# Kernel optimization log

Measured on AMD Instinct MI355X. Metric: run time of the kernel, lower is better.

Reference implementation:

```python
import jax, jax.numpy as jnp
import numpy as np

N_NODES = 50000
N_EDGES = 800000
N_GRAPHS = 512
IN_C, HID, OUT_C = 128, 256, 16


def _mlp(h, w1, b1, w2, b2):
    # PyG-style 2-layer MLP: Linear -> ReLU -> Linear (plain last layer)
    return jax.nn.relu(h @ w1 + b1) @ w2 + b2


def setup_inputs() -> dict:
    key = jax.random.key(0)
    ks = jax.random.split(key, 16)
    x = jax.random.normal(ks[0], (N_NODES, IN_C), dtype=jnp.float32)
    edge_index = jax.random.randint(ks[1], (2, N_EDGES), 0, N_NODES, dtype=jnp.int64)
    batch = jnp.sort(jax.random.randint(ks[2], (N_NODES,), 0, N_GRAPHS, dtype=jnp.int64))

    def lin(k, fan_in, fan_out):
        s = 1.0 / np.sqrt(fan_in)
        return jax.random.uniform(k, (fan_in, fan_out), jnp.float32, -s, s)

    inp = {"x": x, "edge_index": edge_index, "batch": batch}
    dims = [(IN_C, HID), (HID, HID), (HID, HID)]
    ki = 3
    for li, (din, dh) in enumerate(dims):
        inp[f"c{li}_w1"] = lin(ks[ki], din, dh); ki += 1
        inp[f"c{li}_b1"] = jnp.zeros((dh,), jnp.float32)
        inp[f"c{li}_w2"] = lin(ks[ki], dh, dh); ki += 1
        inp[f"c{li}_b2"] = jnp.zeros((dh,), jnp.float32)
    inp["out_w1"] = lin(ks[ki], HID, HID); ki += 1
    inp["out_b1"] = jnp.zeros((HID,), jnp.float32)
    inp["out_w2"] = lin(ks[ki], HID, OUT_C); ki += 1
    inp["out_b2"] = jnp.zeros((OUT_C,), jnp.float32)
    return inp


def reference(x, edge_index, batch,
              c0_w1, c0_b1, c0_w2, c0_b2,
              c1_w1, c1_b1, c1_w2, c1_b2,
              c2_w1, c2_b1, c2_w2, c2_b2,
              out_w1, out_b1, out_w2, out_b2):
    src, dst = edge_index[0], edge_index[1]
    params = [(c0_w1, c0_b1, c0_w2, c0_b2),
              (c1_w1, c1_b1, c1_w2, c1_b2),
              (c2_w1, c2_b1, c2_w2, c2_b2)]
    h = x
    for (w1, b1, w2, b2) in params:
        # GINConv with eps=0: MLP(x + sum_{j in N(i)} x_j)
        agg = jax.ops.segment_sum(h[src], dst, num_segments=N_NODES)
        h = _mlp(h + agg, w1, b1, w2, b2)
        h = jax.nn.relu(h)
        # dropout: identity (eval mode)
    # global mean pool over graphs
    sums = jax.ops.segment_sum(h, batch, num_segments=N_GRAPHS)
    counts = jax.ops.segment_sum(jnp.ones((N_NODES,), h.dtype), batch, num_segments=N_GRAPHS)
    pooled = sums / jnp.maximum(counts, 1.0)[:, None]
    return _mlp(pooled, out_w1, out_b1, out_w2, out_b2)
```

## Files before the change

### kernel.cpp

```cpp
#include <hip/hip_runtime.h>

#define N_NODES 50000
#define N_EDGES 800000
#define N_GRAPHS 512
#define IN_C 128
#define HID 256
#define OUT_C 16

typedef __attribute__((ext_vector_type(8))) short short8;
typedef __attribute__((ext_vector_type(4))) float f32x4;

__device__ __forceinline__ float bf2f(unsigned short u) {
    return __uint_as_float(((unsigned int)u) << 16);
}
__device__ __forceinline__ unsigned short f2bf(float f) {
    unsigned int u = __float_as_uint(f);
    u += 0x7fff + ((u >> 16) & 1);
    return (unsigned short)(u >> 16);
}

#define PLANE_ELEMS ((long)N_NODES * 32)

struct PrepArgs {
    const float* x;
    const float* w[6];
    ushort* xbf;
    ushort* wt[6];
    int* deg;
    float* sums;
};

__global__ __launch_bounds__(256) void prep_kernel(PrepArgs a) {
    const int X4    = N_NODES * IN_C / 4;
    const int TW    = IN_C * HID;
    const int TH    = HID * HID;
    const int TBASE = X4;
    const int TEND  = TBASE + TW + 5 * TH;
    const int D4    = N_NODES / 4;
    const int DBASE = TEND;
    const int SBASE = DBASE + D4;
    const int S4    = N_GRAPHS * HID / 4;
    const long total = (long)SBASE + S4;

    long stride = (long)gridDim.x * blockDim.x;
    for (long i = (long)blockIdx.x * blockDim.x + threadIdx.x; i < total; i += stride) {
        if (i < X4) {
            float4 v = ((const float4*)a.x)[i];
            ushort4 o;
            o.x = f2bf(v.x); o.y = f2bf(v.y); o.z = f2bf(v.z); o.w = f2bf(v.w);
            long e = i * 4;
            int node = (int)(e >> 7);
            int col  = (int)(e & 127);
            long off = (long)(col >> 5) * PLANE_ELEMS + (long)node * 32 + (col & 31);
            *(ushort4*)(a.xbf + off) = o;
        } else if (i < TEND) {
            long r = i - TBASE;
            int wi, shift;
            long off;
            if (r < TW) { wi = 0; shift = 7; off = r; }
            else { r -= TW; wi = 1 + (int)(r / TH); shift = 8; off = r % TH; }
            int n = (int)(off >> shift);
            int k = (int)(off - ((long)n << shift));
            a.wt[wi][off] = f2bf(a.w[wi][(long)k * HID + n]);
        } else if (i < SBASE) {
            ((int4*)a.deg)[i - DBASE] = make_int4(0, 0, 0, 0);
        } else {
            ((float4*)a.sums)[i - SBASE] = make_float4(0.f, 0.f, 0.f, 0.f);
        }
    }
}

__global__ void deg_rank_kernel(const int* __restrict__ dst, int* __restrict__ deg,
                                int* __restrict__ rank) {
    int e = blockIdx.x * blockDim.x + threadIdx.x;
    if (e < N_EDGES) rank[e] = atomicAdd(&deg[dst[e]], 1);
}

__global__ __launch_bounds__(256) void scan_block(const int* __restrict__ deg,
                                                  int* __restrict__ partial,
                                                  int* __restrict__ blockSums) {
    __shared__ int s[256];
    int t = threadIdx.x;
    int i = blockIdx.x * 256 + t;
    int v = (i < N_NODES) ? deg[i] : 0;
    s[t] = v;
    __syncthreads();
    #pragma unroll
    for (int off = 1; off < 256; off <<= 1) {
        int add = (t >= off) ? s[t - off] : 0;
        __syncthreads();
        s[t] += add;
        __syncthreads();
    }
    if (i < N_NODES) partial[i] = s[t] - v;
    if (t == 255) blockSums[blockIdx.x] = s[255];
}

__global__ __launch_bounds__(256) void add_offsets_fused(
    const int* __restrict__ partial, const int* __restrict__ blockSums,
    int* __restrict__ rowptr, int nb) {
    __shared__ int s[256];
    __shared__ int myOff;
    int t = threadIdx.x;
    int v = (t < nb) ? blockSums[t] : 0;
    s[t] = v;
    __syncthreads();
    #pragma unroll
    for (int off = 1; off < 256; off <<= 1) {
        int add = (t >= off) ? s[t - off] : 0;
        __syncthreads();
        s[t] += add;
        __syncthreads();
    }
    if (t == blockIdx.x) myOff = s[t] - v;
    __syncthreads();
    int i = blockIdx.x * 256 + t;
    if (i < N_NODES) rowptr[i] = partial[i] + myOff;
    if (i == 0) rowptr[N_NODES] = N_EDGES;
}

#define NSHARD 8
#define SHARD_SZ ((N_NODES + NSHARD - 1) / NSHARD)
#define EDGES_PER_BLK 2048

__global__ __launch_bounds__(256) void scatter_edges_sharded(
    const int* __restrict__ src, const int* __restrict__ dst,
    const int* __restrict__ rank, const int* __restrict__ rowptr,
    int* __restrict__ srcSorted) {
    int b = blockIdx.x;
    int shard = b & 7;
    int chunk = b >> 3;
    int lo = shard * SHARD_SZ;
    int hi = lo + SHARD_SZ;
    int base = chunk * EDGES_PER_BLK + threadIdx.x;
    #pragma unroll
    for (int u = 0; u < EDGES_PER_BLK / 256; ++u) {
        int e = base + u * 256;
        if (e < N_EDGES) {
            int d = dst[e];
            if (d >= lo && d < hi)
                srcSorted[rowptr[d] + rank[e]] = src[e];
        }
    }
}

template <int C>
__global__ __launch_bounds__(256) void gin_aggregate_planar(
    const ushort* __restrict__ hp,
    const int* __restrict__ rowptr,
    const int* __restrict__ srcIdx,
    ushort* __restrict__ out)
{
    constexpr int NC  = C / 32;
    constexpr int PER = 8 / NC;

    int b  = blockIdx.x;
    int x8 = b & 7;
    int chunk   = x8 / PER;
    int nodeblk = (b >> 3) * PER + (x8 & (PER - 1));

    int lane = threadIdx.x & 63;
    int wave = threadIdx.x >> 6;
    int grp  = lane >> 2;
    int l    = lane & 3;
    int node = nodeblk * 64 + wave * 16 + grp;
    if (node >= N_NODES) return;

    const ushort* plane = hp + (long)chunk * PLANE_ELEMS + l * 8;

    float acc[8];
    {
        short8 sv = *(const short8*)(plane + (long)node * 32);
        #pragma unroll
        for (int v = 0; v < 8; ++v) acc[v] = bf2f((unsigned short)sv[v]);
    }

    int beg = rowptr[node], end = rowptr[node + 1];
    int k = beg;
    for (; k + 8 <= end; k += 8) {
        int si[8];
        #pragma unroll
        for (int u = 0; u < 8; ++u) si[u] = srcIdx[k + u];
        short8 r[8];
        #pragma unroll
        for (int u = 0; u < 8; ++u) r[u] = *(const short8*)(plane + (long)si[u] * 32);
        #pragma unroll
        for (int u = 0; u < 8; ++u)
            #pragma unroll
            for (int v = 0; v < 8; ++v) acc[v] += bf2f((unsigned short)r[u][v]);
    }
    for (; k + 2 <= end; k += 2) {
        int si0 = srcIdx[k], si1 = srcIdx[k + 1];
        short8 r0 = *(const short8*)(plane + (long)si0 * 32);
        short8 r1 = *(const short8*)(plane + (long)si1 * 32);
        #pragma unroll
        for (int v = 0; v < 8; ++v) acc[v] += bf2f((unsigned short)r0[v]);
        #pragma unroll
        for (int v = 0; v < 8; ++v) acc[v] += bf2f((unsigned short)r1[v]);
    }
    if (k < end) {
        short8 r = *(const short8*)(plane + (long)srcIdx[k] * 32);
        #pragma unroll
        for (int v = 0; v < 8; ++v) acc[v] += bf2f((unsigned short)r[v]);
    }

    short8 o;
    #pragma unroll
    for (int v = 0; v < 8; ++v) o[v] = (short)f2bf(acc[v]);
    __builtin_nontemporal_store(o, (short8*)(out + (long)node * C + chunk * 32 + l * 8));
}

template <int K1, bool FUSE_POOL>
__global__ __launch_bounds__(512, 2) void gin_mlp_persist(
    const ushort* __restrict__ A,
    const ushort* __restrict__ w1t,
    const float* __restrict__ b1,
    const ushort* __restrict__ w2t,
    const float* __restrict__ b2,
    ushort* __restrict__ out,
    const int* __restrict__ batch,
    float* __restrict__ sums,
    int M, int nTiles, int nPers)
{
    constexpr int NCH1 = K1 / 8;
    constexpr int NSLOT1 = 64 * NCH1;
    constexpr int NS1 = K1 / 32;
    constexpr int PFN = NSLOT1 / 512;

    __shared__ short LsA[NSLOT1 * 8];
    __shared__ short LsH[2048 * 8];

    int t = threadIdx.x;
    int lane = t & 63;
    int wv = t >> 6;
    int quad = lane >> 4;
    int l15 = lane & 15;
    int swz = l15 & 7;
    int col0 = wv * 32;

    short8 w1r[NS1 * 2];
    #pragma unroll
    for (int s = 0; s < NS1; ++s)
        #pragma unroll
        for (int j = 0; j < 2; ++j)
            w1r[s * 2 + j] = *(const short8*)(w1t + (long)(col0 + j * 16 + l15) * K1 + s * 32 + quad * 8);
    short8 w2r[16];
    #pragma unroll
    for (int s = 0; s < 8; ++s)
        #pragma unroll
        for (int j = 0; j < 2; ++j)
            w2r[s * 2 + j] = *(const short8*)(w2t + (long)(col0 + j * 16 + l15) * 256 + s * 32 + quad * 8);
    float bv1[2], bv2[2];
    #pragma unroll
    for (int j = 0; j < 2; ++j) {
        bv1[j] = b1[col0 + j * 16 + l15];
        bv2[j] = b2[col0 + j * 16 + l15];
    }

    int t0 = (int)(((long)blockIdx.x * nTiles) / nPers);
    int t1 = (int)(((long)(blockIdx.x + 1) * nTiles) / nPers);

    const f32x4 zero = {0.f, 0.f, 0.f, 0.f};

    for (int ti = t0; ti < t1; ++ti) {
        int row0 = ti * 64;

        #pragma unroll
        for (int c = 0; c < PFN; ++c) {
            int s = c * 512 + t;
            int row = s / NCH1;
            int kcs = s & (NCH1 - 1);
            int kc = kcs ^ (row & 7);
            int grow = row0 + row;
            if (grow >= M) grow = M - 1;
            *(short8*)&LsA[s * 8] = *(const short8*)(A + (long)grow * K1 + kc * 8);
        }
        __syncthreads();

        f32x4 acc[4][2];
        #pragma unroll
        for (int i = 0; i < 4; ++i)
            #pragma unroll
            for (int j = 0; j < 2; ++j) acc[i][j] = zero;

        #pragma unroll
        for (int s = 0; s < NS1; ++s) {
            #pragma unroll
            for (int i = 0; i < 4; ++i) {
                int row = i * 16 + l15;
                int slot = row * NCH1 + ((s * 4 + quad) ^ swz);
                short8 a = *(const short8*)&LsA[slot * 8];
                acc[i][0] = __builtin_amdgcn_mfma_f32_16x16x32_bf16(a, w1r[s * 2 + 0], acc[i][0], 0, 0, 0);
                acc[i][1] = __builtin_amdgcn_mfma_f32_16x16x32_bf16(a, w1r[s * 2 + 1], acc[i][1], 0, 0, 0);
            }
        }
        __syncthreads();

        #pragma unroll
        for (int i = 0; i < 4; ++i)
            #pragma unroll
            for (int j = 0; j < 2; ++j) {
                int col = col0 + j * 16 + l15;
                int kc2 = col >> 3, sub = col & 7;
                #pragma unroll
                for (int r = 0; r < 4; ++r) {
                    int row = i * 16 + quad * 4 + r;
                    int slot = row * 32 + (kc2 ^ (row & 7));
                    float o = fmaxf(acc[i][j][r] + bv1[j], 0.f);
                    LsH[slot * 8 + sub] = (short)f2bf(o);
                }
            }
        __syncthreads();

        #pragma unroll
        for (int i = 0; i < 4; ++i)
            #pragma unroll
            for (int j = 0; j < 2; ++j) acc[i][j] = zero;

        #pragma unroll
        for (int s = 0; s < 8; ++s) {
            #pragma unroll
            for (int i = 0; i < 4; ++i) {
                int row = i * 16 + l15;
                int slot = row * 32 + ((s * 4 + quad) ^ swz);
                short8 a = *(const short8*)&LsH[slot * 8];
                acc[i][0] = __builtin_amdgcn_mfma_f32_16x16x32_bf16(a, w2r[s * 2 + 0], acc[i][0], 0, 0, 0);
                acc[i][1] = __builtin_amdgcn_mfma_f32_16x16x32_bf16(a, w2r[s * 2 + 1], acc[i][1], 0, 0, 0);
            }
        }

        if constexpr (!FUSE_POOL) {
            #pragma unroll
            for (int i = 0; i < 4; ++i)
                #pragma unroll
                for (int r = 0; r < 4; ++r) {
                    int grow = row0 + i * 16 + quad * 4 + r;
                    if (grow >= M) continue;
                    #pragma unroll
                    for (int j = 0; j < 2; ++j) {
                        int col = col0 + j * 16 + l15;
                        float o = fmaxf(acc[i][j][r] + bv2[j], 0.f);
                        out[(long)(col >> 5) * PLANE_ELEMS + (long)grow * 32 + (col & 31)] = f2bf(o);
                    }
                }
        } else {
            float pacc[2];
            #pragma unroll
            for (int j = 0; j < 2; ++j) pacc[j] = 0.f;
            int cur = -1;
            #pragma unroll
            for (int i = 0; i < 4; ++i) {
                #pragma unroll
                for (int r = 0; r < 4; ++r) {
                    int row = row0 + i * 16 + quad * 4 + r;
                    if (row >= M) continue;
                    int g = batch[row];
                    if (g != cur) {
                        if (cur >= 0) {
                            #pragma unroll
                            for (int j = 0; j < 2; ++j)
                                atomicAdd(&sums[(long)cur * 256 + col0 + j * 16 + l15], pacc[j]);
                        }
                        cur = g;
                        #pragma unroll
                        for (int j = 0; j < 2; ++j) pacc[j] = 0.f;
                    }
                    #pragma unroll
                    for (int j = 0; j < 2; ++j)
                        pacc[j] += fmaxf(acc[i][j][r] + bv2[j], 0.f);
                }
            }
            if (cur >= 0) {
                #pragma unroll
                for (int j = 0; j < 2; ++j)
                    atomicAdd(&sums[(long)cur * 256 + col0 + j * 16 + l15], pacc[j]);
            }
        }
    }
}

__global__ __launch_bounds__(256) void final_mlp_kernel(
    const float* __restrict__ sums, const int* __restrict__ batch,
    const float* __restrict__ w1, const float* __restrict__ b1,
    const float* __restrict__ w2, const float* __restrict__ b2,
    float* __restrict__ out) {
    __shared__ float row[HID];
    __shared__ float hid[HID];
    __shared__ int cntS;
    int g = blockIdx.x;
    int t = threadIdx.x;
    if (t == 0) {
        int lo = 0, hi = N_NODES;
        while (lo < hi) { int m = (lo + hi) >> 1; if (batch[m] < g) lo = m + 1; else hi = m; }
        int lo2 = lo, hi2 = N_NODES;
        while (lo2 < hi2) { int m = (lo2 + hi2) >> 1; if (batch[m] < g + 1) lo2 = m + 1; else hi2 = m; }
        cntS = lo2 - lo;
    }
    __syncthreads();
    float cnt = fmaxf((float)cntS, 1.0f);
    row[t] = sums[(long)g * HID + t] / cnt;
    __syncthreads();
    float acc = b1[t];
    for (int k = 0; k < HID; ++k) acc += row[k] * w1[k * HID + t];
    hid[t] = fmaxf(acc, 0.f);
    __syncthreads();
    if (t < OUT_C) {
        float o = b2[t];
        for (int k = 0; k < HID; ++k) o += hid[k] * w2[k * OUT_C + t];
        out[(long)g * OUT_C + t] = o;
    }
}

extern "C" void kernel_launch(void* const* d_in, const int* in_sizes, int n_in,
                              void* d_out, int out_size, void* d_ws, size_t ws_size,
                              hipStream_t stream) {
    const float* x     = (const float*)d_in[0];
    const int*   ei    = (const int*)d_in[1];
    const int*   batch = (const int*)d_in[2];
    const int*   src   = ei;
    const int*   dst   = ei + N_EDGES;

    const float* c_w1[3] = { (const float*)d_in[3],  (const float*)d_in[7],  (const float*)d_in[11] };
    const float* c_b1[3] = { (const float*)d_in[4],  (const float*)d_in[8],  (const float*)d_in[12] };
    const float* c_w2[3] = { (const float*)d_in[5],  (const float*)d_in[9],  (const float*)d_in[13] };
    const float* c_b2[3] = { (const float*)d_in[6],  (const float*)d_in[10], (const float*)d_in[14] };
    const float* out_w1 = (const float*)d_in[15];
    const float* out_b1 = (const float*)d_in[16];
    const float* out_w2 = (const float*)d_in[17];
    const float* out_b2 = (const float*)d_in[18];

    char* p = (char*)d_ws;
    auto alloc = [&](size_t bytes) {
        char* r = p;
        p += (bytes + 15) & ~(size_t)15;
        return r;
    };
    ushort* xbf  = (ushort*)alloc((size_t)N_NODES * IN_C * 2);
    ushort* bufA = (ushort*)alloc((size_t)N_NODES * HID * 2);
    ushort* bufB = (ushort*)alloc((size_t)N_NODES * HID * 2);
    ushort* wt[6];
    wt[0] = (ushort*)alloc((size_t)IN_C * HID * 2);
    for (int i = 1; i < 6; ++i) wt[i] = (ushort*)alloc((size_t)HID * HID * 2);
    float* sums   = (float*)alloc((size_t)N_GRAPHS * HID * 4);
    int* deg       = (int*)alloc((size_t)N_NODES * 4);
    int* rowptr    = (int*)alloc((size_t)(N_NODES + 1) * 4);
    int* blockSums = (int*)alloc(256 * 4);
    int* rank      = (int*)alloc((size_t)N_EDGES * 4);
    int* srcSorted = (int*)alloc((size_t)N_EDGES * 4);

    const int nb = (N_NODES + 255) / 256;

    {
        PrepArgs a;
        a.x = x;
        a.w[0] = c_w1[0]; a.w[1] = c_w2[0];
        a.w[2] = c_w1[1]; a.w[3] = c_w2[1];
        a.w[4] = c_w1[2]; a.w[5] = c_w2[2];
        a.xbf = xbf;
        for (int i = 0; i < 6; ++i) a.wt[i] = wt[i];
        a.deg = deg;
        a.sums = sums;
        prep_kernel<<<2048, 256, 0, stream>>>(a);
    }

    deg_rank_kernel<<<(N_EDGES + 255) / 256, 256, 0, stream>>>(dst, deg, rank);
    scan_block<<<nb, 256, 0, stream>>>(deg, rowptr, blockSums);
    add_offsets_fused<<<nb, 256, 0, stream>>>(rowptr, blockSums, rowptr, nb);
    {
        const int chunks = (N_EDGES + EDGES_PER_BLK - 1) / EDGES_PER_BLK;
        scatter_edges_sharded<<<chunks * NSHARD, 256, 0, stream>>>(src, dst, rank, rowptr, srcSorted);
    }

    const int nodeBlks = (N_NODES + 63) / 64;
    const int aggX128  = nodeBlks * (IN_C / 32);
    const int aggX256  = nodeBlks * (HID / 32);
    const int NPERS    = 256;

    gin_aggregate_planar<IN_C><<<aggX128, 256, 0, stream>>>(xbf, rowptr, srcSorted, bufB);
    gin_mlp_persist<IN_C, false><<<NPERS, 512, 0, stream>>>(bufB, wt[0], c_b1[0], wt[1], c_b2[0],
                                                            bufA, batch, sums, N_NODES, nodeBlks, NPERS);

    gin_aggregate_planar<HID><<<aggX256, 256, 0, stream>>>(bufA, rowptr, srcSorted, bufB);
    gin_mlp_persist<HID, false><<<NPERS, 512, 0, stream>>>(bufB, wt[2], c_b1[1], wt[3], c_b2[1],
                                                           bufA, batch, sums, N_NODES, nodeBlks, NPERS);

    gin_aggregate_planar<HID><<<aggX256, 256, 0, stream>>>(bufA, rowptr, srcSorted, bufB);
    gin_mlp_persist<HID, true><<<NPERS, 512, 0, stream>>>(bufB, wt[4], c_b1[2], wt[5], c_b2[2],
                                                          bufA, batch, sums, N_NODES, nodeBlks, NPERS);

    final_mlp_kernel<<<N_GRAPHS, 256, 0, stream>>>(sums, batch, out_w1, out_b1,
                                                   out_w2, out_b2, (float*)d_out);
}
```

Measured before the change: 397.0 us.

## Register-prefetch next A tile during MLP GEMM and pin weights in VGPRs

The persistent MLP kernel now loads the next 64-row tile of A into registers while the current tile is computed, then writes it to LDS at the top of the next iteration. This hides global load latency behind the MFMA work. Per-thread row and swizzle offsets are precomputed once. Empty asm statements force the weight fragments to stay resident in VGPRs. The extra prefetch registers and the pinned weights raise VGPR pressure, which may cut occupancy or cause spills.

After: 396.7 us. About the same (-0.1%).

```diff
diff --git a/kernel.cpp b/kernel.cpp
--- a/kernel.cpp
+++ b/kernel.cpp
@@ -250,6 +250,11 @@
         #pragma unroll
         for (int j = 0; j < 2; ++j)
             w2r[s * 2 + j] = *(const short8*)(w2t + (long)(col0 + j * 16 + l15) * 256 + s * 32 + quad * 8);
+    #pragma unroll
+    for (int i = 0; i < NS1 * 2; ++i) asm volatile("" : "+v"(w1r[i]));
+    #pragma unroll
+    for (int i = 0; i < 16; ++i) asm volatile("" : "+v"(w2r[i]));
+
     float bv1[2], bv2[2];
     #pragma unroll
     for (int j = 0; j < 2; ++j) {
@@ -257,23 +262,46 @@
         bv2[j] = b2[col0 + j * 16 + l15];
     }
 
+    int prow[PFN], pkcB[PFN];
+    #pragma unroll
+    for (int c = 0; c < PFN; ++c) {
+        int s = c * 512 + t;
+        prow[c] = s / NCH1;
+        int kcs = s & (NCH1 - 1);
+        pkcB[c] = (kcs ^ (prow[c] & 7)) * 8;
+    }
+
     int t0 = (int)(((long)blockIdx.x * nTiles) / nPers);
     int t1 = (int)(((long)(blockIdx.x + 1) * nTiles) / nPers);
+    if (t0 >= t1) return;
 
     const f32x4 zero = {0.f, 0.f, 0.f, 0.f};
+
+    short8 pf[PFN];
+    {
+        int row0 = t0 * 64;
+        #pragma unroll
+        for (int c = 0; c < PFN; ++c) {
+            int grow = row0 + prow[c];
+            if (grow >= M) grow = M - 1;
+            pf[c] = *(const short8*)(A + (long)grow * K1 + pkcB[c]);
+        }
+    }
 
     for (int ti = t0; ti < t1; ++ti) {
         int row0 = ti * 64;
 
         #pragma unroll
-        for (int c = 0; c < PFN; ++c) {
-            int s = c * 512 + t;
-            int row = s / NCH1;
-            int kcs = s & (NCH1 - 1);
-            int kc = kcs ^ (row & 7);
-            int grow = row0 + row;
-            if (grow >= M) grow = M - 1;
-            *(short8*)&LsA[s * 8] = *(const short8*)(A + (long)grow * K1 + kc * 8);
+        for (int c = 0; c < PFN; ++c)
+            *(short8*)&LsA[(c * 512 + t) * 8] = pf[c];
+        if (ti + 1 < t1) {
+            int nrow0 = (ti + 1) * 64;
+            #pragma unroll
+            for (int c = 0; c < PFN; ++c) {
+                int grow = nrow0 + prow[c];
+                if (grow >= M) grow = M - 1;
+                pf[c] = *(const short8*)(A + (long)grow * K1 + pkcB[c]);
+            }
         }
         __syncthreads();
 
```
